# Optimization experiments

Measured on AMD Instinct MI355X. Metric: run time of the kernel, lower is better.

The kernel has to match this reference:

```python
import jax, jax.numpy as jnp
import numpy as np

N = 100_000          # nodes
E = 3_200_000        # edges
DIM = 64             # filt_conv_dimension
L = 3                # filt_conv_number
MAX_DEG = 64         # embedding table size = MAX_DEG + 1
SUM_DIMS = DIM * (L + 1)  # 256, fc input
BN_EPS = 1e-5
NEG_SLOPE = 0.01


def _leaky(x):
    return jnp.where(x >= 0, x, NEG_SLOPE * x)


def _batchnorm(x, g, b):
    # training-mode BN over the node axis
    mu = jnp.mean(x, axis=0, keepdims=True)
    var = jnp.var(x, axis=0, keepdims=True)
    return g * (x - mu) * jax.lax.rsqrt(var + BN_EPS) + b


def setup_inputs() -> dict:
    key = jax.random.key(0)
    ks = jax.random.split(key, 16)
    s = 0.05
    inp = {
        "node_deg": jax.random.randint(ks[0], (N,), 0, MAX_DEG, dtype=jnp.int32),
        "edge_index": jax.random.randint(ks[1], (2, E), 0, N, dtype=jnp.int32),
        "embed_deg": jax.random.normal(ks[2], (MAX_DEG + 1, DIM), jnp.float32) * s,
        "eps": jnp.zeros((L,), jnp.float32),
        "W1": jax.random.normal(ks[3], (L, DIM, DIM), jnp.float32) * s,
        "b1": jnp.zeros((L, DIM), jnp.float32),
        "W2": jax.random.normal(ks[4], (L, DIM, DIM), jnp.float32) * s,
        "b2": jnp.zeros((L, DIM), jnp.float32),
        "bn_g": jnp.ones((L, DIM), jnp.float32),
        "bn_b": jnp.zeros((L, DIM), jnp.float32),
        "fc_W1": jax.random.normal(ks[5], (SUM_DIMS, DIM), jnp.float32) * s,
        "fc_b1": jnp.zeros((DIM,), jnp.float32),
        "fc_bn_g": jnp.ones((DIM,), jnp.float32),
        "fc_bn_b": jnp.zeros((DIM,), jnp.float32),
        "fc_W2": jax.random.normal(ks[6], (DIM, 1), jnp.float32) * s,
        "fc_b2": jnp.zeros((1,), jnp.float32),
    }
    return inp


def reference(node_deg, edge_index, embed_deg, eps, W1, b1, W2, b2,
              bn_g, bn_b, fc_W1, fc_b1, fc_bn_g, fc_bn_b, fc_W2, fc_b2):
    src, dst = edge_index[0], edge_index[1]
    h = embed_deg[node_deg]                       # [N, DIM]
    z = [h]
    for l in range(L):
        x = z[-1]
        # GINConv: (1+eps)*x_i + sum_{j->i} x_j, then MLP lin_lrelu_lin
        agg = jax.ops.segment_sum(x[src], dst, num_segments=N)  # [N, DIM]
        m = (1.0 + eps[l]) * x + agg
        h1 = _leaky(m @ W1[l] + b1[l])
        out = h1 @ W2[l] + b2[l]
        out = _leaky(_batchnorm(out, bn_g[l], bn_b[l]))
        z.append(out)
    xcat = jnp.concatenate(z, axis=1)             # [N, SUM_DIMS]
    hfc = _leaky(_batchnorm(xcat @ fc_W1 + fc_b1, fc_bn_g, fc_bn_b))
    ret = jax.nn.sigmoid(hfc @ fc_W2 + fc_b2)     # [N, 1]
    return jnp.squeeze(ret, axis=-1)              # [N]
```

## Files before the change

kernel.cpp:

```cpp
#include <hip/hip_runtime.h>
#include <hip/hip_bf16.h>

#define NN 100000
#define NE 3200000
#define D 64
#define BN_EPS 1e-5f

#define NP 512
#define CHUNK 6250
#define NB 391
#define SPREAD 16

typedef float v2f __attribute__((ext_vector_type(2)));

#define FMA4(accr, xs, w4) \
  accr.x += (xs) * (w4).x; accr.y += (xs) * (w4).y; \
  accr.z += (xs) * (w4).z; accr.w += (xs) * (w4).w;

__global__ __launch_bounds__(256) void bucket_kernel(const int* __restrict__ ei,
    int* __restrict__ rec, int* __restrict__ S) {
  __shared__ int cntL[392];
  __shared__ int curL[392];
  __shared__ int scanbuf[256];
  int t = threadIdx.x;
  int p = blockIdx.x;
  int e0 = p * CHUNK;
  cntL[t] = 0;
  if (t < 136) cntL[256 + t] = 0;
  __syncthreads();
  for (int e = t; e < CHUNK; e += 256) {
    int dd = ei[NE + e0 + e];
    atomicAdd(&cntL[(unsigned)dd >> 8], 1);
  }
  __syncthreads();
  int a0 = 0, a1 = 0;
  if (t < 196) { a0 = cntL[2 * t]; a1 = cntL[2 * t + 1]; }
  int s = a0 + a1;
  scanbuf[t] = s;
  __syncthreads();
  for (int off = 1; off < 256; off <<= 1) {
    int x = (t >= off) ? scanbuf[t - off] : 0;
    __syncthreads();
    scanbuf[t] += x;
    __syncthreads();
  }
  int ex = scanbuf[t] - s;
  if (t < 196) {
    curL[2 * t]     = ex;
    curL[2 * t + 1] = ex + a0;
    S[p * 392 + 2 * t]     = e0 + ex;
    S[p * 392 + 2 * t + 1] = e0 + ex + a0;
  }
  __syncthreads();
  for (int e = t; e < CHUNK; e += 256) {
    int ss = ei[e0 + e];
    int dd = ei[NE + e0 + e];
    int b = (unsigned)dd >> 8;
    int pos = atomicAdd(&curL[b], 1);
    rec[e0 + pos] = ss | ((dd & 255) << 17);
  }
}

__global__ __launch_bounds__(256) void bucketsum_kernel(const int* __restrict__ S,
    int* __restrict__ bsum) {
  __shared__ int sh[256];
  int B = blockIdx.x;
  int t = threadIdx.x;
  int c = 0;
  for (int p = t; p < NP; p += 256)
    c += S[p * 392 + B + 1] - S[p * 392 + B];
  sh[t] = c;
  __syncthreads();
  for (int o = 128; o > 0; o >>= 1) {
    if (t < o) sh[t] += sh[t + o];
    __syncthreads();
  }
  if (t == 0) bsum[B] = sh[0];
}

__global__ __launch_bounds__(512) void scan2_kernel(int* __restrict__ bsum) {
  __shared__ int sh[512];
  int t = threadIdx.x;
  int v = (t < NB) ? bsum[t] : 0;
  sh[t] = v;
  __syncthreads();
  for (int o = 1; o < 512; o <<= 1) {
    int x = (t >= o) ? sh[t - o] : 0;
    __syncthreads();
    sh[t] += x;
    __syncthreads();
  }
  if (t < NB) bsum[t] = sh[t] - v;
}

__global__ __launch_bounds__(512) void sort_kernel(const int* __restrict__ rec,
    const int* __restrict__ S, const int* __restrict__ bsum,
    const int* __restrict__ deg,
    int* __restrict__ csroff, int* __restrict__ csrsrc,
    unsigned* __restrict__ cnt8) {
  __shared__ int cntL[256];
  __shared__ int curL[256];
  __shared__ unsigned hist[256 * 65];
  int t = threadIdx.x;
  int B = blockIdx.x;
  if (t < 256) cntL[t] = 0;
  for (int k = t; k < 256 * 65; k += 512) hist[k] = 0;
  __syncthreads();
  int lane = t & 15;
  int g = t >> 4;
  for (int p = g; p < NP; p += 32) {
    int s0 = S[p * 392 + B], s1 = S[p * 392 + B + 1];
    for (int e = s0 + lane; e < s1; e += 16) {
      int r = rec[e];
      int dl = (unsigned)r >> 17;
      atomicAdd(&cntL[dl], 1);
      atomicAdd(&hist[dl * 65 + deg[r & 0x1FFFF]], 1u);
    }
  }
  __syncthreads();
  int v = 0;
  if (t < 256) { v = cntL[t]; curL[t] = v; }
  __syncthreads();
  for (int o = 1; o < 256; o <<= 1) {
    int x = 0;
    if (t < 256 && t >= o) x = curL[t - o];
    __syncthreads();
    if (t < 256) curL[t] += x;
    __syncthreads();
  }
  int b0 = bsum[B];
  if (t < 256) {
    int excl = curL[t] - v;
    int node = B * 256 + t;
    if (node <= NN) csroff[node] = b0 + excl;
  }
  __syncthreads();
  if (t < 256) curL[t] = b0 + (curL[t] - v);
  if (t < 256) {
    int node = B * 256 + t;
    if (node < NN) {
      #pragma unroll
      for (int j = 0; j < 16; j++) {
        unsigned p = (hist[t * 65 + 4 * j] & 255)
                   | ((hist[t * 65 + 4 * j + 1] & 255) << 8)
                   | ((hist[t * 65 + 4 * j + 2] & 255) << 16)
                   | ((hist[t * 65 + 4 * j + 3] & 255) << 24);
        cnt8[(long)node * 16 + j] = p;
      }
    }
  }
  __syncthreads();
  for (int p = g; p < NP; p += 32) {
    int s0 = S[p * 392 + B], s1 = S[p * 392 + B + 1];
    for (int e = s0 + lane; e < s1; e += 16) {
      int r = rec[e];
      int pos = atomicAdd(&curL[(unsigned)r >> 17], 1);
      csrsrc[pos] = r & 0x1FFFF;
    }
  }
}

__global__ __launch_bounds__(256) void agg_kernel(const int* __restrict__ off,
    const int* __restrict__ srcs, const unsigned* __restrict__ xh32,
    float* __restrict__ agg) {
  int t = threadIdx.x;
  int lane = t & 7;
  int g = t >> 3;
  int b = blockIdx.x;
  int slice = b & 1;
  int i = (b >> 1) * 32 + g;
  const unsigned* base = xh32 + (long)slice * NN * 8;
  int e0 = off[i], e1 = off[i + 1];
  float s0 = 0.f, s1 = 0.f, s2 = 0.f, s3 = 0.f;
  int e = e0;
  for (; e + 4 <= e1; e += 4) {
    int j0 = srcs[e + 0], j1 = srcs[e + 1], j2 = srcs[e + 2], j3 = srcs[e + 3];
    unsigned u0 = base[(long)j0 * 8 + lane];
    unsigned u1 = base[(long)j1 * 8 + lane];
    unsigned u2 = base[(long)j2 * 8 + lane];
    unsigned u3 = base[(long)j3 * 8 + lane];
    v2f l0 = __builtin_amdgcn_cvt_pk_f32_fp8((int)u0, false);
    v2f h0 = __builtin_amdgcn_cvt_pk_f32_fp8((int)u0, true);
    v2f l1 = __builtin_amdgcn_cvt_pk_f32_fp8((int)u1, false);
    v2f h1 = __builtin_amdgcn_cvt_pk_f32_fp8((int)u1, true);
    v2f l2 = __builtin_amdgcn_cvt_pk_f32_fp8((int)u2, false);
    v2f h2 = __builtin_amdgcn_cvt_pk_f32_fp8((int)u2, true);
    v2f l3 = __builtin_amdgcn_cvt_pk_f32_fp8((int)u3, false);
    v2f h3 = __builtin_amdgcn_cvt_pk_f32_fp8((int)u3, true);
    s0 += (l0.x + l1.x) + (l2.x + l3.x);
    s1 += (l0.y + l1.y) + (l2.y + l3.y);
    s2 += (h0.x + h1.x) + (h2.x + h3.x);
    s3 += (h0.y + h1.y) + (h2.y + h3.y);
  }
  for (; e < e1; e++) {
    unsigned u = base[(long)srcs[e] * 8 + lane];
    v2f lo = __builtin_amdgcn_cvt_pk_f32_fp8((int)u, false);
    v2f hi = __builtin_amdgcn_cvt_pk_f32_fp8((int)u, true);
    s0 += lo.x; s1 += lo.y; s2 += hi.x; s3 += hi.y;
  }
  *(float4*)&agg[(long)i * D + slice * 32 + lane * 4] = make_float4(s0, s1, s2, s3);
}

__global__ __launch_bounds__(256) void layer_kernel(
    const float* __restrict__ X,
    const float* __restrict__ AGG,
    const unsigned* __restrict__ CNT8, const float* __restrict__ EMB,
    const int* __restrict__ deg, float* __restrict__ Z0,
    const float* __restrict__ epsv, int l,
    const float* __restrict__ W1, const float* __restrict__ b1,
    const float* __restrict__ W2, const float* __restrict__ b2,
    float* __restrict__ Z, float* __restrict__ spread)
{
  __shared__ float Ws[64][64];
  __shared__ float XsT[64][128];
  int t = threadIdx.x;
  int i0 = blockIdx.x * 128;
  float alpha = 1.0f + epsv[l];
  int c0 = (t & 15) * 4;
  int r0 = (t >> 4) * 8;
  int wr = t >> 4;
  int wc = (t & 15) * 4;
  int row = t & 127;
  int gi_row = i0 + row;
  int gis_row = (gi_row < NN) ? gi_row : NN - 1;
  int kb = (t >> 7) * 32;

  if (CNT8) {
    #pragma unroll
    for (int j = 0; j < 4; j++)
      *(float4*)&Ws[wr + 16 * j][wc] = *(const float4*)&EMB[(long)(wr + 16 * j) * D + wc];
    #pragma unroll
    for (int j = 0; j < 8; j++) {
      unsigned u = CNT8[(long)gis_row * 16 + (kb >> 2) + j];
      int k = kb + 4 * j;
      XsT[k + 0][row] = (float)(u & 255);
      XsT[k + 1][row] = (float)((u >> 8) & 255);
      XsT[k + 2][row] = (float)((u >> 16) & 255);
      XsT[k + 3][row] = (float)(u >> 24);
    }
    __syncthreads();
    float4 acc[8];
    #pragma unroll
    for (int r = 0; r < 8; r++) acc[r] = make_float4(0.f, 0.f, 0.f, 0.f);
    #pragma unroll 4
    for (int k = 0; k < 64; k++) {
      float4 w4 = *(const float4*)&Ws[k][c0];
      float4 xa = *(const float4*)&XsT[k][r0];
      float4 xb = *(const float4*)&XsT[k][r0 + 4];
      FMA4(acc[0], xa.x, w4); FMA4(acc[1], xa.y, w4);
      FMA4(acc[2], xa.z, w4); FMA4(acc[3], xa.w, w4);
      FMA4(acc[4], xb.x, w4); FMA4(acc[5], xb.y, w4);
      FMA4(acc[6], xb.z, w4); FMA4(acc[7], xb.w, w4);
    }
    __syncthreads();
    #pragma unroll
    for (int r = 0; r < 8; r++) {
      int gi = i0 + r0 + r;
      int gis = (gi < NN) ? gi : NN - 1;
      float4 xv = *(const float4*)&EMB[(long)deg[gis] * D + c0];
      if (gi < NN) *(float4*)&Z0[(long)gi * 256 + c0] = xv;
      XsT[c0 + 0][r0 + r] = alpha * xv.x + acc[r].x;
      XsT[c0 + 1][r0 + r] = alpha * xv.y + acc[r].y;
      XsT[c0 + 2][r0 + r] = alpha * xv.z + acc[r].z;
      XsT[c0 + 3][r0 + r] = alpha * xv.w + acc[r].w;
    }
    #pragma unroll
    for (int j = 0; j < 4; j++)
      *(float4*)&Ws[wr + 16 * j][wc] = *(const float4*)&W1[(long)(wr + 16 * j) * D + wc];
    __syncthreads();
  } else {
    #pragma unroll
    for (int j = 0; j < 4; j++)
      *(float4*)&Ws[wr + 16 * j][wc] = *(const float4*)&W1[(long)(wr + 16 * j) * D + wc];
    #pragma unroll
    for (int j = 0; j < 8; j++) {
      int k = kb + 4 * j;
      float4 xv = *(const float4*)&X[(long)gis_row * 256 + k];
      float4 a4 = *(const float4*)&AGG[(long)gis_row * D + k];
      XsT[k + 0][row] = alpha * xv.x + a4.x;
      XsT[k + 1][row] = alpha * xv.y + a4.y;
      XsT[k + 2][row] = alpha * xv.z + a4.z;
      XsT[k + 3][row] = alpha * xv.w + a4.w;
    }
    __syncthreads();
  }

  float4 h[8];
  {
    float4 b4 = *(const float4*)&b1[c0];
    #pragma unroll
    for (int r = 0; r < 8; r++) h[r] = b4;
  }
  #pragma unroll 4
  for (int k = 0; k < 64; k++) {
    float4 w4 = *(const float4*)&Ws[k][c0];
    float4 xa = *(const float4*)&XsT[k][r0];
    float4 xb = *(const float4*)&XsT[k][r0 + 4];
    FMA4(h[0], xa.x, w4); FMA4(h[1], xa.y, w4);
    FMA4(h[2], xa.z, w4); FMA4(h[3], xa.w, w4);
    FMA4(h[4], xb.x, w4); FMA4(h[5], xb.y, w4);
    FMA4(h[6], xb.z, w4); FMA4(h[7], xb.w, w4);
  }
  #pragma unroll
  for (int r = 0; r < 8; r++) {
    h[r].x = (h[r].x >= 0.0f) ? h[r].x : 0.01f * h[r].x;
    h[r].y = (h[r].y >= 0.0f) ? h[r].y : 0.01f * h[r].y;
    h[r].z = (h[r].z >= 0.0f) ? h[r].z : 0.01f * h[r].z;
    h[r].w = (h[r].w >= 0.0f) ? h[r].w : 0.01f * h[r].w;
  }
  __syncthreads();
  #pragma unroll
  for (int r = 0; r < 8; r++) {
    XsT[c0 + 0][r0 + r] = h[r].x;
    XsT[c0 + 1][r0 + r] = h[r].y;
    XsT[c0 + 2][r0 + r] = h[r].z;
    XsT[c0 + 3][r0 + r] = h[r].w;
  }
  #pragma unroll
  for (int j = 0; j < 4; j++)
    *(float4*)&Ws[wr + 16 * j][wc] = *(const float4*)&W2[(long)(wr + 16 * j) * D + wc];
  __syncthreads();

  float4 z[8];
  {
    float4 b4 = *(const float4*)&b2[c0];
    #pragma unroll
    for (int r = 0; r < 8; r++) z[r] = b4;
  }
  #pragma unroll 4
  for (int k = 0; k < 64; k++) {
    float4 w4 = *(const float4*)&Ws[k][c0];
    float4 xa = *(const float4*)&XsT[k][r0];
    float4 xb = *(const float4*)&XsT[k][r0 + 4];
    FMA4(z[0], xa.x, w4); FMA4(z[1], xa.y, w4);
    FMA4(z[2], xa.z, w4); FMA4(z[3], xa.w, w4);
    FMA4(z[4], xb.x, w4); FMA4(z[5], xb.y, w4);
    FMA4(z[6], xb.z, w4); FMA4(z[7], xb.w, w4);
  }
  #pragma unroll
  for (int r = 0; r < 8; r++) {
    int gi = i0 + r0 + r;
    if (gi < NN) *(float4*)&Z[(long)gi * 256 + c0] = z[r];
  }

  float s[4] = {0, 0, 0, 0}, sq[4] = {0, 0, 0, 0};
  #pragma unroll
  for (int r = 0; r < 8; r++) {
    if (i0 + r0 + r < NN) {
      s[0] += z[r].x; sq[0] += z[r].x * z[r].x;
      s[1] += z[r].y; sq[1] += z[r].y * z[r].y;
      s[2] += z[r].z; sq[2] += z[r].z * z[r].z;
      s[3] += z[r].w; sq[3] += z[r].w * z[r].w;
    }
  }
  __syncthreads();
  float* red = &XsT[0][0];
  int grp = t >> 4;
  #pragma unroll
  for (int j = 0; j < 4; j++) {
    red[grp * 64 + c0 + j] = s[j];
    red[1024 + grp * 64 + c0 + j] = sq[j];
  }
  __syncthreads();
  if (t < 64) {
    float a = 0.0f, b = 0.0f;
    #pragma unroll
    for (int g = 0; g < 16; g++) {
      a += red[g * 64 + t];
      b += red[1024 + g * 64 + t];
    }
    int slot = blockIdx.x & (SPREAD - 1);
    atomicAdd(&spread[slot * 128 + t], a);
    atomicAdd(&spread[slot * 128 + 64 + t], b);
  }
}

__global__ __launch_bounds__(256) void fc1_kernel(
    const float* __restrict__ X,
    const float* __restrict__ W, const float* __restrict__ bias,
    float* __restrict__ Y, float* __restrict__ spread)
{
  __shared__ float Ws[64][64];
  __shared__ float XsT[64][128];
  int t = threadIdx.x;
  int i0 = blockIdx.x * 128;
  int c0 = (t & 15) * 4;
  int r0 = (t >> 4) * 8;
  int wr = t >> 4;
  int wc = (t & 15) * 4;
  int row = t & 127;
  int gi_row = i0 + row;
  int gis_row = (gi_row < NN) ? gi_row : NN - 1;
  int kb = (t >> 7) * 32;

  float4 acc[8];
  {
    float4 b4 = *(const float4*)&bias[c0];
    #pragma unroll
    for (int r = 0; r < 8; r++) acc[r] = b4;
  }
  for (int kc = 0; kc < 256; kc += 64) {
    __syncthreads();
    #pragma unroll
    for (int j = 0; j < 4; j++)
      *(float4*)&Ws[wr + 16 * j][wc] = *(const float4*)&W[(long)(kc + wr + 16 * j) * D + wc];
    #pragma unroll
    for (int j = 0; j < 8; j++) {
      int k = kb + 4 * j;
      float4 xv = *(const float4*)&X[(long)gis_row * 256 + kc + k];
      XsT[k + 0][row] = xv.x;
      XsT[k + 1][row] = xv.y;
      XsT[k + 2][row] = xv.z;
      XsT[k + 3][row] = xv.w;
    }
    __syncthreads();
    #pragma unroll 4
    for (int k = 0; k < 64; k++) {
      float4 w4 = *(const float4*)&Ws[k][c0];
      float4 xa = *(const float4*)&XsT[k][r0];
      float4 xb = *(const float4*)&XsT[k][r0 + 4];
      FMA4(acc[0], xa.x, w4); FMA4(acc[1], xa.y, w4);
      FMA4(acc[2], xa.z, w4); FMA4(acc[3], xa.w, w4);
      FMA4(acc[4], xb.x, w4); FMA4(acc[5], xb.y, w4);
      FMA4(acc[6], xb.z, w4); FMA4(acc[7], xb.w, w4);
    }
  }
  #pragma unroll
  for (int r = 0; r < 8; r++) {
    int gi = i0 + r0 + r;
    if (gi < NN) *(float4*)&Y[(long)gi * D + c0] = acc[r];
  }
  float s[4] = {0, 0, 0, 0}, sq[4] = {0, 0, 0, 0};
  #pragma unroll
  for (int r = 0; r < 8; r++) {
    if (i0 + r0 + r < NN) {
      s[0] += acc[r].x; sq[0] += acc[r].x * acc[r].x;
      s[1] += acc[r].y; sq[1] += acc[r].y * acc[r].y;
      s[2] += acc[r].z; sq[2] += acc[r].z * acc[r].z;
      s[3] += acc[r].w; sq[3] += acc[r].w * acc[r].w;
    }
  }
  __syncthreads();
  float* red = &XsT[0][0];
  int grp = t >> 4;
  #pragma unroll
  for (int j = 0; j < 4; j++) {
    red[grp * 64 + c0 + j] = s[j];
    red[1024 + grp * 64 + c0 + j] = sq[j];
  }
  __syncthreads();
  if (t < 64) {
    float a = 0.0f, b = 0.0f;
    #pragma unroll
    for (int g = 0; g < 16; g++) {
      a += red[g * 64 + t];
      b += red[1024 + g * 64 + t];
    }
    int slot = blockIdx.x & (SPREAD - 1);
    atomicAdd(&spread[slot * 128 + t], a);
    atomicAdd(&spread[slot * 128 + 64 + t], b);
  }
}

__global__ __launch_bounds__(128) void bn_finalize_kernel(
    const float* __restrict__ spread, float* __restrict__ statsF) {
  int t = threadIdx.x;
  float a = 0.0f;
  #pragma unroll
  for (int g = 0; g < SPREAD; g++) a += spread[g * 128 + t];
  statsF[t] = a;
}

__global__ __launch_bounds__(256) void bn_apply_kernel(float* __restrict__ Zs,
    const float* __restrict__ stats,
    const float* __restrict__ g, const float* __restrict__ b,
    unsigned short* __restrict__ Outh) {
  int idx = blockIdx.x * 256 + threadIdx.x;
  int i = idx >> 5, dp = (idx & 31) * 2;
  if (i >= NN) return;
  float invn = 1.0f / (float)NN;
  float v0, v1;
  {
    float mu = stats[dp] * invn;
    float var = fmaxf(stats[64 + dp] * invn - mu * mu, 0.0f);
    float sc = g[dp] * rsqrtf(var + BN_EPS);
    v0 = sc * (Zs[(long)i * 256 + dp] - mu) + b[dp];
    v0 = (v0 >= 0.0f) ? v0 : 0.01f * v0;
  }
  {
    float mu = stats[dp + 1] * invn;
    float var = fmaxf(stats[64 + dp + 1] * invn - mu * mu, 0.0f);
    float sc = g[dp + 1] * rsqrtf(var + BN_EPS);
    v1 = sc * (Zs[(long)i * 256 + dp + 1] - mu) + b[dp + 1];
    v1 = (v1 >= 0.0f) ? v1 : 0.01f * v1;
  }
  Zs[(long)i * 256 + dp]     = v0;
  Zs[(long)i * 256 + dp + 1] = v1;
  if (Outh) {
    int packed = __builtin_amdgcn_cvt_pk_fp8_f32(v0, v1, 0, false);
    Outh[(long)(dp >> 5) * NN * 16 + (long)i * 16 + ((dp & 31) >> 1)] =
        (unsigned short)packed;
  }
}

__global__ __launch_bounds__(256) void fc2bn_kernel(const float* __restrict__ H,
    const float* __restrict__ stats,
    const float* __restrict__ g, const float* __restrict__ b,
    const float* __restrict__ W2, const float* __restrict__ b2,
    float* __restrict__ out) {
  int tid = threadIdx.x;
  int k = tid & 63, q = tid >> 6;
  int i = blockIdx.x * 4 + q;
  float invn = 1.0f / (float)NN;
  float mu = stats[k] * invn;
  float var = fmaxf(stats[64 + k] * invn - mu * mu, 0.0f);
  float sc = g[k] * rsqrtf(var + BN_EPS);
  float v = 0.0f;
  if (i < NN) {
    float hv = sc * (H[(long)i * D + k] - mu) + b[k];
    hv = (hv >= 0.0f) ? hv : 0.01f * hv;
    v = hv * W2[k];
  }
  #pragma unroll
  for (int off = 32; off > 0; off >>= 1)
    v += __shfl_down(v, off);
  if (k == 0 && i < NN) {
    float x = v + b2[0];
    out[i] = 1.0f / (1.0f + __expf(-x));
  }
}

extern "C" void kernel_launch(void* const* d_in, const int* in_sizes, int n_in,
                              void* d_out, int out_size, void* d_ws, size_t ws_size,
                              hipStream_t stream) {
  const int*   node_deg   = (const int*)d_in[0];
  const int*   edge_index = (const int*)d_in[1];
  const float* embedw     = (const float*)d_in[2];
  const float* eps        = (const float*)d_in[3];
  const float* W1         = (const float*)d_in[4];
  const float* b1         = (const float*)d_in[5];
  const float* W2         = (const float*)d_in[6];
  const float* b2         = (const float*)d_in[7];
  const float* bn_g       = (const float*)d_in[8];
  const float* bn_b       = (const float*)d_in[9];
  const float* fc_W1      = (const float*)d_in[10];
  const float* fc_b1      = (const float*)d_in[11];
  const float* fc_bn_g    = (const float*)d_in[12];
  const float* fc_bn_b    = (const float*)d_in[13];
  const float* fc_W2      = (const float*)d_in[14];
  const float* fc_b2      = (const float*)d_in[15];

  float* zcat   = (float*)d_ws;
  float* agg    = zcat + (long)NN * 256;
  float* statsS = agg + (long)NN * D;
  float* statsF = statsS + 4 * SPREAD * 128;
  int*   csroff = (int*)(statsF + 512);
  int*   bsum   = csroff + NN + 1;
  int*   csrsrc = bsum + 512;
  int*   rec    = csrsrc + NE;
  int*   S      = rec + NE;
  unsigned* cnt8 = (unsigned*)(S + NP * 392);
  unsigned short* xh = (unsigned short*)rec;

  const int rowBlocks   = NN / 4;
  const int layerBlocks = (NN + 127) / 128;
  const int aggBlocks   = (NN / 32) * 2;
  const int bnBlocks    = (NN * 32 + 255) / 256;

  bucket_kernel<<<NP, 256, 0, stream>>>(edge_index, rec, S);
  bucketsum_kernel<<<NB, 256, 0, stream>>>(S, bsum);
  scan2_kernel<<<1, 512, 0, stream>>>(bsum);
  sort_kernel<<<NB, 512, 0, stream>>>(rec, S, bsum, node_deg,
      csroff, csrsrc, cnt8);

  hipMemsetAsync(statsS, 0, (size_t)(4 * SPREAD * 128 + 512) * sizeof(float), stream);

  for (int l = 0; l < 3; ++l) {
    if (l > 0)
      agg_kernel<<<aggBlocks, 256, 0, stream>>>(csroff, csrsrc,
          (const unsigned*)xh, agg);
    layer_kernel<<<layerBlocks, 256, 0, stream>>>(zcat + l * D,
        (l == 0) ? nullptr : agg,
        (l == 0) ? cnt8 : nullptr, embedw, node_deg, zcat,
        eps, l,
        W1 + (long)l * D * D, b1 + (long)l * D,
        W2 + (long)l * D * D, b2 + (long)l * D,
        zcat + (l + 1) * D, statsS + (long)l * SPREAD * 128);
    bn_finalize_kernel<<<1, 128, 0, stream>>>(statsS + (long)l * SPREAD * 128,
        statsF + (long)l * 128);
    bn_apply_kernel<<<bnBlocks, 256, 0, stream>>>(zcat + (l + 1) * D,
        statsF + (long)l * 128, bn_g + (long)l * D, bn_b + (long)l * D,
        (l < 2) ? xh : nullptr);
  }

  fc1_kernel<<<layerBlocks, 256, 0, stream>>>(zcat, fc_W1, fc_b1, agg,
      statsS + 3L * SPREAD * 128);
  bn_finalize_kernel<<<1, 128, 0, stream>>>(statsS + 3L * SPREAD * 128,
      statsF + 3L * 128);
  fc2bn_kernel<<<rowBlocks, 256, 0, stream>>>(agg, statsF + 3L * 128,
      fc_bn_g, fc_bn_b, fc_W2, fc_b2, (float*)d_out);
}
```

Baseline: 537.0 us.

## Unslice fp8 feature layout in aggregation and shrink layer tiles to 64 rows

The aggregation kernel no longer splits the 64 fp8 features into two 32-wide slices handled by separate blocks. Each node's row is now stored contiguously (64 bytes) and gathered by 16 lanes, so every neighbor index is read once instead of twice. Separately, the layer and fc1 GEMM kernels move from 128-row to 64-row tiles with 4 rows per thread. This halves shared memory and register use to raise occupancy and block count, at the cost of less weight reuse per block.

After: 515.5 us. 4.0% less time.

```diff
diff --git a/kernel.cpp b/kernel.cpp
--- a/kernel.cpp
+++ b/kernel.cpp
@@ -164,21 +164,18 @@
     const int* __restrict__ srcs, const unsigned* __restrict__ xh32,
     float* __restrict__ agg) {
   int t = threadIdx.x;
-  int lane = t & 7;
-  int g = t >> 3;
-  int b = blockIdx.x;
-  int slice = b & 1;
-  int i = (b >> 1) * 32 + g;
-  const unsigned* base = xh32 + (long)slice * NN * 8;
+  int lane = t & 15;
+  int g = t >> 4;
+  int i = blockIdx.x * 16 + g;
   int e0 = off[i], e1 = off[i + 1];
   float s0 = 0.f, s1 = 0.f, s2 = 0.f, s3 = 0.f;
   int e = e0;
   for (; e + 4 <= e1; e += 4) {
     int j0 = srcs[e + 0], j1 = srcs[e + 1], j2 = srcs[e + 2], j3 = srcs[e + 3];
-    unsigned u0 = base[(long)j0 * 8 + lane];
-    unsigned u1 = base[(long)j1 * 8 + lane];
-    unsigned u2 = base[(long)j2 * 8 + lane];
-    unsigned u3 = base[(long)j3 * 8 + lane];
+    unsigned u0 = xh32[(long)j0 * 16 + lane];
+    unsigned u1 = xh32[(long)j1 * 16 + lane];
+    unsigned u2 = xh32[(long)j2 * 16 + lane];
+    unsigned u3 = xh32[(long)j3 * 16 + lane];
     v2f l0 = __builtin_amdgcn_cvt_pk_f32_fp8((int)u0, false);
     v2f h0 = __builtin_amdgcn_cvt_pk_f32_fp8((int)u0, true);
     v2f l1 = __builtin_amdgcn_cvt_pk_f32_fp8((int)u1, false);
@@ -193,12 +190,12 @@
     s3 += (h0.y + h1.y) + (h2.y + h3.y);
   }
   for (; e < e1; e++) {
-    unsigned u = base[(long)srcs[e] * 8 + lane];
+    unsigned u = xh32[(long)srcs[e] * 16 + lane];
     v2f lo = __builtin_amdgcn_cvt_pk_f32_fp8((int)u, false);
     v2f hi = __builtin_amdgcn_cvt_pk_f32_fp8((int)u, true);
     s0 += lo.x; s1 += lo.y; s2 += hi.x; s3 += hi.y;
   }
-  *(float4*)&agg[(long)i * D + slice * 32 + lane * 4] = make_float4(s0, s1, s2, s3);
+  *(float4*)&agg[(long)i * D + lane * 4] = make_float4(s0, s1, s2, s3);
 }
 
 __global__ __launch_bounds__(256) void layer_kernel(
@@ -212,25 +209,25 @@
     float* __restrict__ Z, float* __restrict__ spread)
 {
   __shared__ float Ws[64][64];
-  __shared__ float XsT[64][128];
-  int t = threadIdx.x;
-  int i0 = blockIdx.x * 128;
+  __shared__ float XsT[64][64];
+  int t = threadIdx.x;
+  int i0 = blockIdx.x * 64;
   float alpha = 1.0f + epsv[l];
   int c0 = (t & 15) * 4;
-  int r0 = (t >> 4) * 8;
+  int r0 = (t >> 4) * 4;
   int wr = t >> 4;
   int wc = (t & 15) * 4;
-  int row = t & 127;
+  int row = t & 63;
   int gi_row = i0 + row;
   int gis_row = (gi_row < NN) ? gi_row : NN - 1;
-  int kb = (t >> 7) * 32;
+  int kb = (t >> 6) * 16;
 
   if (CNT8) {
     #pragma unroll
     for (int j = 0; j < 4; j++)
       *(float4*)&Ws[wr + 16 * j][wc] = *(const float4*)&EMB[(long)(wr + 16 * j) * D + wc];
     #pragma unroll
-    for (int j = 0; j < 8; j++) {
+    for (int j = 0; j < 4; j++) {
       unsigned u = CNT8[(long)gis_row * 16 + (kb >> 2) + j];
       int k = kb + 4 * j;
       XsT[k + 0][row] = (float)(u & 255);
@@ -239,22 +236,19 @@
       XsT[k + 3][row] = (float)(u >> 24);
     }
     __syncthreads();
-    float4 acc[8];
-    #pragma unroll
-    for (int r = 0; r < 8; r++) acc[r] = make_float4(0.f, 0.f, 0.f, 0.f);
-    #pragma unroll 4
+    float4 acc[4];
+    #pragma unroll
+    for (int r = 0; r < 4; r++) acc[r] = make_float4(0.f, 0.f, 0.f, 0.f);
+    #pragma unroll 8
     for (int k = 0; k < 64; k++) {
       float4 w4 = *(const float4*)&Ws[k][c0];
-      float4 xa = *(const float4*)&XsT[k][r0];
-      float4 xb = *(const float4*)&XsT[k][r0 + 4];
-      FMA4(acc[0], xa.x, w4); FMA4(acc[1], xa.y, w4);
-      FMA4(acc[2], xa.z, w4); FMA4(acc[3], xa.w, w4);
-      FMA4(acc[4], xb.x, w4); FMA4(acc[5], xb.y, w4);
-      FMA4(acc[6], xb.z, w4); FMA4(acc[7], xb.w, w4);
-    }
-    __syncthreads();
-    #pragma unroll
-    for (int r = 0; r < 8; r++) {
+      float4 x4 = *(const float4*)&XsT[k][r0];
+      FMA4(acc[0], x4.x, w4); FMA4(acc[1], x4.y, w4);
+      FMA4(acc[2], x4.z, w4); FMA4(acc[3], x4.w, w4);
+    }
+    __syncthreads();
+    #pragma unroll
+    for (int r = 0; r < 4; r++) {
       int gi = i0 + r0 + r;
       int gis = (gi < NN) ? gi : NN - 1;
       float4 xv = *(const float4*)&EMB[(long)deg[gis] * D + c0];
@@ -273,7 +267,7 @@
     for (int j = 0; j < 4; j++)
       *(float4*)&Ws[wr + 16 * j][wc] = *(const float4*)&W1[(long)(wr + 16 * j) * D + wc];
     #pragma unroll
-    for (int j = 0; j < 8; j++) {
+    for (int j = 0; j < 4; j++) {
       int k = kb + 4 * j;
       float4 xv = *(const float4*)&X[(long)gis_row * 256 + k];
       float4 a4 = *(const float4*)&AGG[(long)gis_row * D + k];
@@ -285,24 +279,21 @@
     __syncthreads();
   }
 
-  float4 h[8];
+  float4 h[4];
   {
     float4 b4 = *(const float4*)&b1[c0];
     #pragma unroll
-    for (int r = 0; r < 8; r++) h[r] = b4;
-  }
-  #pragma unroll 4
+    for (int r = 0; r < 4; r++) h[r] = b4;
+  }
+  #pragma unroll 8
   for (int k = 0; k < 64; k++) {
     float4 w4 = *(const float4*)&Ws[k][c0];
-    float4 xa = *(const float4*)&XsT[k][r0];
-    float4 xb = *(const float4*)&XsT[k][r0 + 4];
-    FMA4(h[0], xa.x, w4); FMA4(h[1], xa.y, w4);
-    FMA4(h[2], xa.z, w4); FMA4(h[3], xa.w, w4);
-    FMA4(h[4], xb.x, w4); FMA4(h[5], xb.y, w4);
-    FMA4(h[6], xb.z, w4); FMA4(h[7], xb.w, w4);
-  }
-  #pragma unroll
-  for (int r = 0; r < 8; r++) {
+    float4 x4 = *(const float4*)&XsT[k][r0];
+    FMA4(h[0], x4.x, w4); FMA4(h[1], x4.y, w4);
+    FMA4(h[2], x4.z, w4); FMA4(h[3], x4.w, w4);
+  }
+  #pragma unroll
+  for (int r = 0; r < 4; r++) {
     h[r].x = (h[r].x >= 0.0f) ? h[r].x : 0.01f * h[r].x;
     h[r].y = (h[r].y >= 0.0f) ? h[r].y : 0.01f * h[r].y;
     h[r].z = (h[r].z >= 0.0f) ? h[r].z : 0.01f * h[r].z;
@@ -310,7 +301,7 @@
   }
   __syncthreads();
   #pragma unroll
-  for (int r = 0; r < 8; r++) {
+  for (int r = 0; r < 4; r++) {
     XsT[c0 + 0][r0 + r] = h[r].x;
     XsT[c0 + 1][r0 + r] = h[r].y;
     XsT[c0 + 2][r0 + r] = h[r].z;
@@ -321,31 +312,28 @@
     *(float4*)&Ws[wr + 16 * j][wc] = *(const float4*)&W2[(long)(wr + 16 * j) * D + wc];
   __syncthreads();
 
-  float4 z[8];
+  float4 z[4];
   {
     float4 b4 = *(const float4*)&b2[c0];
     #pragma unroll
-    for (int r = 0; r < 8; r++) z[r] = b4;
-  }
-  #pragma unroll 4
+    for (int r = 0; r < 4; r++) z[r] = b4;
+  }
+  #pragma unroll 8
   for (int k = 0; k < 64; k++) {
     float4 w4 = *(const float4*)&Ws[k][c0];
-    float4 xa = *(const float4*)&XsT[k][r0];
-    float4 xb = *(const float4*)&XsT[k][r0 + 4];
-    FMA4(z[0], xa.x, w4); FMA4(z[1], xa.y, w4);
-    FMA4(z[2], xa.z, w4); FMA4(z[3], xa.w, w4);
-    FMA4(z[4], xb.x, w4); FMA4(z[5], xb.y, w4);
-    FMA4(z[6], xb.z, w4); FMA4(z[7], xb.w, w4);
-  }
-  #pragma unroll
-  for (int r = 0; r < 8; r++) {
+    float4 x4 = *(const float4*)&XsT[k][r0];
+    FMA4(z[0], x4.x, w4); FMA4(z[1], x4.y, w4);
+    FMA4(z[2], x4.z, w4); FMA4(z[3], x4.w, w4);
+  }
+  #pragma unroll
+  for (int r = 0; r < 4; r++) {
     int gi = i0 + r0 + r;
     if (gi < NN) *(float4*)&Z[(long)gi * 256 + c0] = z[r];
   }
 
   float s[4] = {0, 0, 0, 0}, sq[4] = {0, 0, 0, 0};
   #pragma unroll
-  for (int r = 0; r < 8; r++) {
+  for (int r = 0; r < 4; r++) {
     if (i0 + r0 + r < NN) {
       s[0] += z[r].x; sq[0] += z[r].x * z[r].x;
       s[1] += z[r].y; sq[1] += z[r].y * z[r].y;
@@ -381,58 +369,57 @@
     float* __restrict__ Y, float* __restrict__ spread)
 {
   __shared__ float Ws[64][64];
-  __shared__ float XsT[64][128];
-  int t = threadIdx.x;
-  int i0 = blockIdx.x * 128;
+  __shared__ float XsT[64][64];
+  int t = threadIdx.x;
+  int i0 = blockIdx.x * 64;
   int c0 = (t & 15) * 4;
-  int r0 = (t >> 4) * 8;
+  int r0 = (t >> 4) * 4;
   int wr = t >> 4;
   int wc = (t & 15) * 4;
-  int row = t & 127;
-  int gi_row = i0 + row;
-  int gis_row = (gi_row < NN) ? gi_row : NN - 1;
-  int kb = (t >> 7) * 32;
-
-  float4 acc[8];
+
+  float4 acc[4];
   {
     float4 b4 = *(const float4*)&bias[c0];
     #pragma unroll
-    for (int r = 0; r < 8; r++) acc[r] = b4;
+    for (int r = 0; r < 4; r++) acc[r] = b4;
   }
   for (int kc = 0; kc < 256; kc += 64) {
     __syncthreads();
     #pragma unroll
     for (int j = 0; j < 4; j++)
       *(float4*)&Ws[wr + 16 * j][wc] = *(const float4*)&W[(long)(kc + wr + 16 * j) * D + wc];
-    #pragma unroll
-    for (int j = 0; j < 8; j++) {
-      int k = kb + 4 * j;
-      float4 xv = *(const float4*)&X[(long)gis_row * 256 + kc + k];
-      XsT[k + 0][row] = xv.x;
-      XsT[k + 1][row] = xv.y;
-      XsT[k + 2][row] = xv.z;
-      XsT[k + 3][row] = xv.w;
-    }
-    __syncthreads();
-    #pragma unroll 4
+    {
+      int row = t & 63;
+      int gi = i0 + row;
+      int gis = (gi < NN) ? gi : NN - 1;
+      int kb = (t >> 6) * 16;
+      #pragma unroll
+      for (int j = 0; j < 4; j++) {
+        int k = kb + 4 * j;
+        float4 xv = *(const float4*)&X[(long)gis * 256 + kc + k];
+        XsT[k + 0][row] = xv.x;
+        XsT[k + 1][row] = xv.y;
+        XsT[k + 2][row] = xv.z;
+        XsT[k + 3][row] = xv.w;
+      }
+    }
+    __syncthreads();
+    #pragma unroll 8
     for (int k = 0; k < 64; k++) {
       float4 w4 = *(const float4*)&Ws[k][c0];
-      float4 xa = *(const float4*)&XsT[k][r0];
-      float4 xb = *(const float4*)&XsT[k][r0 + 4];
-      FMA4(acc[0], xa.x, w4); FMA4(acc[1], xa.y, w4);
-      FMA4(acc[2], xa.z, w4); FMA4(acc[3], xa.w, w4);
-      FMA4(acc[4], xb.x, w4); FMA4(acc[5], xb.y, w4);
-      FMA4(acc[6], xb.z, w4); FMA4(acc[7], xb.w, w4);
-    }
-  }
-  #pragma unroll
-  for (int r = 0; r < 8; r++) {
+      float4 x4 = *(const float4*)&XsT[k][r0];
+      FMA4(acc[0], x4.x, w4); FMA4(acc[1], x4.y, w4);
+      FMA4(acc[2], x4.z, w4); FMA4(acc[3], x4.w, w4);
+    }
+  }
+  #pragma unroll
+  for (int r = 0; r < 4; r++) {
     int gi = i0 + r0 + r;
     if (gi < NN) *(float4*)&Y[(long)gi * D + c0] = acc[r];
   }
   float s[4] = {0, 0, 0, 0}, sq[4] = {0, 0, 0, 0};
   #pragma unroll
-  for (int r = 0; r < 8; r++) {
+  for (int r = 0; r < 4; r++) {
     if (i0 + r0 + r < NN) {
       s[0] += acc[r].x; sq[0] += acc[r].x * acc[r].x;
       s[1] += acc[r].y; sq[1] += acc[r].y * acc[r].y;
@@ -498,8 +485,7 @@
   Zs[(long)i * 256 + dp + 1] = v1;
   if (Outh) {
     int packed = __builtin_amdgcn_cvt_pk_fp8_f32(v0, v1, 0, false);
-    Outh[(long)(dp >> 5) * NN * 16 + (long)i * 16 + ((dp & 31) >> 1)] =
-        (unsigned short)packed;
+    Outh[(long)i * 32 + (dp >> 1)] = (unsigned short)packed;
   }
 }
 
@@ -563,8 +549,8 @@
   unsigned short* xh = (unsigned short*)rec;
 
   const int rowBlocks   = NN / 4;
-  const int layerBlocks = (NN + 127) / 128;
-  const int aggBlocks   = (NN / 32) * 2;
+  const int layerBlocks = (NN + 63) / 64;
+  const int aggBlocks   = NN / 16;
   const int bnBlocks    = (NN * 32 + 255) / 256;
 
   bucket_kernel<<<NP, 256, 0, stream>>>(edge_index, rec, S);
```
